# Kernel tuning notes

Hardware: AMD Instinct MI355X
Metric: run time of the kernel (lower is better)

Reference implementation:

```python
import jax, jax.numpy as jnp
import numpy as np

NUM_HEADS = 12
HEAD_DIM = 64


def setup_inputs() -> dict:
    key = jax.random.key(0)
    ks = jax.random.split(key, 4)
    B, T, C = 2, 2048, 768
    x = jax.random.normal(ks[0], (B, T, C), dtype=jnp.float32)
    attention_mask = jnp.ones((B, 1, 1, T), dtype=jnp.int32)
    W_attn = jax.random.normal(ks[1], (C, 3 * C), dtype=jnp.float32) * 0.02
    b_attn = jnp.zeros((3 * C,), dtype=jnp.float32)
    W_proj = jax.random.normal(ks[2], (C, C), dtype=jnp.float32) * 0.02
    b_proj = jnp.zeros((C,), dtype=jnp.float32)
    return {"x": x, "attention_mask": attention_mask, "W_attn": W_attn,
            "b_attn": b_attn, "W_proj": W_proj, "b_proj": b_proj}


def reference(x, attention_mask, W_attn, b_attn, W_proj, b_proj):
    B, T, C = x.shape
    H, D = NUM_HEADS, HEAD_DIM
    # c_attn (Conv1D): y = x @ W + b -> [B, T, 3C]
    qkv = x @ W_attn + b_attn
    q, k, v = jnp.split(qkv, 3, axis=-1)
    # [B, T, C] -> [B, H, T, D]
    q = q.reshape(B, T, H, D).transpose(0, 2, 1, 3)
    k = k.reshape(B, T, H, D).transpose(0, 2, 1, 3)
    v = v.reshape(B, T, H, D).transpose(0, 2, 1, 3)
    scores = jnp.einsum('bhqd,bhkd->bhqk', q, k) / jnp.sqrt(jnp.float32(D))
    causal = jnp.tril(jnp.ones((T, T), dtype=bool))[None, None]  # [1,1,T,T]
    mask_value = jnp.finfo(scores.dtype).min
    scores = jnp.where(causal, scores, mask_value)
    scores = jnp.where(attention_mask == 0, -jnp.inf, scores)
    probs = jax.nn.softmax(scores, axis=-1)
    attn_out = jnp.einsum('bhqk,bhkd->bhqd', probs, v)
    attn_out = attn_out.transpose(0, 2, 1, 3).reshape(B, T, C)
    return attn_out @ W_proj + b_proj
```

## Files before the change

### kernel.cpp

```cpp
#include <hip/hip_runtime.h>

typedef __attribute__((ext_vector_type(8))) short bf16x8;
typedef __attribute__((ext_vector_type(4))) float f32x4;
typedef __attribute__((ext_vector_type(16))) float f32x16;

#define MFMA16(a, b, c) __builtin_amdgcn_mfma_f32_16x16x32_bf16(a, b, c, 0, 0, 0)
#define MFMA32(a, b, c) __builtin_amdgcn_mfma_f32_32x32x16_bf16(a, b, c, 0, 0, 0)
#define LOG2E 1.4426950408889634f

#define BB 2
#define TT 2048
#define CC 768
#define HH 12
#define DD 64
#define MM (BB * TT)
#define N1 (3 * CC)

#define BH_STRIDE 131072

static __device__ __forceinline__ unsigned short f2bf(float f) {
  union { float f; unsigned u; } v; v.f = f;
  unsigned r = (v.u + 0x7FFFu + ((v.u >> 16) & 1u)) >> 16;
  return (unsigned short)r;
}

static __device__ __forceinline__ unsigned cvt_pk_bf16(float lo, float hi) {
  unsigned r;
  asm("v_cvt_pk_bf16_f32 %0, %1, %2" : "=v"(r) : "v"(lo), "v"(hi));
  return r;
}

static __device__ __forceinline__ void gload_lds16(const void* g, void* l) {
  __builtin_amdgcn_global_load_lds(
      (const __attribute__((address_space(1))) void*)g,
      (__attribute__((address_space(3))) void*)l, 16, 0, 0);
}

__global__ __launch_bounds__(256) void k_cvt(const float* __restrict__ x,
                                             unsigned short* __restrict__ o) {
  int i = blockIdx.x * 256 + threadIdx.x;
  float4 v = reinterpret_cast<const float4*>(x)[i];
  ushort4 r;
  r.x = f2bf(v.x); r.y = f2bf(v.y); r.z = f2bf(v.z); r.w = f2bf(v.w);
  reinterpret_cast<ushort4*>(o)[i] = r;
}

__global__ __launch_bounds__(128) void k_mbits(const int* __restrict__ mask,
                                               unsigned int* __restrict__ mb) {
  int i = threadIdx.x;
  unsigned bits = 0;
  const int* p = mask + i * 32;
#pragma unroll
  for (int j = 0; j < 32; ++j) bits |= (p[j] != 0 ? 1u : 0u) << j;
  mb[i] = bits;
}

__global__ __launch_bounds__(256) void k_tr(const float* __restrict__ W,
                                            unsigned short* __restrict__ Wt,
                                            int K, int N) {
  __shared__ float tile[32][33];
  int tx = threadIdx.x, ty = threadIdx.y;
  int n0 = blockIdx.x * 32, k0 = blockIdx.y * 32;
#pragma unroll
  for (int i = 0; i < 4; ++i)
    tile[ty + i * 8][tx] = W[(size_t)(k0 + ty + i * 8) * N + n0 + tx];
  __syncthreads();
#pragma unroll
  for (int i = 0; i < 4; ++i)
    Wt[(size_t)(n0 + ty + i * 8) * K + k0 + tx] = f2bf(tile[tx][ty + i * 8]);
}

template <int MODE>
__global__ __launch_bounds__(256) void k_gemm(
    const unsigned short* __restrict__ A, const unsigned short* __restrict__ Bt,
    const float* __restrict__ bias, float* __restrict__ Cout, int N, int K,
    unsigned short* __restrict__ Qb, unsigned short* __restrict__ Kb,
    unsigned short* __restrict__ Vt) {
  __shared__ __align__(16) unsigned short As[128 * 32];
  __shared__ __align__(16) unsigned short Bs[128 * 32];
  const int tid = threadIdx.x;
  const int lane = tid & 63;
  const int wid = tid >> 6;
  const int l15 = lane & 15, l4 = lane >> 4;
  const int wr = wid >> 1, wc = wid & 1;
  const int brow = blockIdx.x * 128, bcol = blockIdx.y * 128;

  f32x4 acc[4][4] = {};

  const int u0 = tid, u1 = tid + 256;
  const int row0 = u0 >> 2, c0 = (u0 & 3) * 8;
  const int row1 = u1 >> 2, c1 = (u1 & 3) * 8;

  const unsigned short* ga0 = A + (size_t)(brow + row0) * K + c0;
  const unsigned short* ga1 = A + (size_t)(brow + row1) * K + c1;
  const unsigned short* gb0 = Bt + (size_t)(bcol + row0) * K + c0;
  const unsigned short* gb1 = Bt + (size_t)(bcol + row1) * K + c1;
  unsigned short* la0 = As + u0 * 8;
  unsigned short* la1 = As + u1 * 8;
  unsigned short* lb0 = Bs + u0 * 8;
  unsigned short* lb1 = Bs + u1 * 8;

  const int NK = K / 32;
  for (int ks = 0; ks < NK; ++ks) {
    if (ks) __syncthreads();
    const int ko = ks * 32;
    gload_lds16(ga0 + ko, la0);
    gload_lds16(ga1 + ko, la1);
    gload_lds16(gb0 + ko, lb0);
    gload_lds16(gb1 + ko, lb1);
    __syncthreads();
    bf16x8 af[4], bfr[4];
#pragma unroll
    for (int mi = 0; mi < 4; ++mi)
      af[mi] = *reinterpret_cast<const bf16x8*>(&As[(wr * 64 + mi * 16 + l15) * 32 + l4 * 8]);
#pragma unroll
    for (int ni = 0; ni < 4; ++ni)
      bfr[ni] = *reinterpret_cast<const bf16x8*>(&Bs[(wc * 64 + ni * 16 + l15) * 32 + l4 * 8]);
#pragma unroll
    for (int mi = 0; mi < 4; ++mi)
#pragma unroll
      for (int ni = 0; ni < 4; ++ni)
        acc[mi][ni] = MFMA16(af[mi], bfr[ni], acc[mi][ni]);
  }

#pragma unroll
  for (int mi = 0; mi < 4; ++mi) {
    const int m0 = brow + wr * 64 + mi * 16 + l4 * 4;
#pragma unroll
    for (int ni = 0; ni < 4; ++ni) {
      const int n = bcol + wc * 64 + ni * 16 + l15;
      const float bv = bias[n];
      if (MODE == 0) {
#pragma unroll
        for (int r = 0; r < 4; ++r)
          Cout[(size_t)(m0 + r) * N + n] = acc[mi][ni][r] + bv;
      } else {
        const int sec = n / CC;
        const int nn = n - sec * CC;
        const int hh = nn >> 6, d = nn & 63;
        const int b = m0 >> 11;
        const int t0 = m0 & 2047;
        const size_t hbase = (size_t)(b * HH + hh) * BH_STRIDE;
        if (sec == 0) {
#pragma unroll
          for (int r = 0; r < 4; ++r) {
            const int t = t0 + r;
            Qb[hbase + ((t >> 5) * 4 + (d >> 4)) * 512 + (t & 31) * 16 + (d & 15)] =
                f2bf((acc[mi][ni][r] + bv) * 0.125f);
          }
        } else if (sec == 1) {
#pragma unroll
          for (int r = 0; r < 4; ++r) {
            const int t = t0 + r;
            Kb[hbase + ((t >> 5) * 4 + (d >> 4)) * 512 + (t & 31) * 16 + (d & 15)] =
                f2bf(acc[mi][ni][r] + bv);
          }
        } else {
          ushort4 pk;
          pk.x = f2bf(acc[mi][ni][0] + bv);
          pk.y = f2bf(acc[mi][ni][1] + bv);
          pk.z = f2bf(acc[mi][ni][2] + bv);
          pk.w = f2bf(acc[mi][ni][3] + bv);
          *reinterpret_cast<ushort4*>(
              &Vt[hbase + ((t0 >> 6) * 4 + ((t0 >> 4) & 3)) * 1024 + d * 16 + (t0 & 15)]) = pk;
        }
      }
    }
  }
}

__device__ __forceinline__ void loadk(bf16x8 (&dst)[2][4], const unsigned short* Kh,
                                      int kv0, int lo) {
  const unsigned short* kp = Kh + (kv0 >> 5) * 2048 + lo;
#pragma unroll
  for (int kg = 0; kg < 2; ++kg)
#pragma unroll
    for (int dg = 0; dg < 4; ++dg)
      dst[kg][dg] = *reinterpret_cast<const bf16x8*>(&kp[kg * 2048 + dg * 512]);
}

__device__ __forceinline__ void attn_tile(
    int kv0, const bf16x8 (&kf)[2][4], uint2 mb, const bf16x8 (&qf)[4],
    const unsigned short* __restrict__ Vh, int q0, int l31, int h, int lo,
    f32x16& o0, f32x16& o1, float& mrow, float& lrow) {
  const unsigned short* vp = Vh + (kv0 >> 6) * 4096 + lo;
  bf16x8 vf0[4], vf1[4];
#pragma unroll
  for (int kc = 0; kc < 4; ++kc) {
    vf0[kc] = *reinterpret_cast<const bf16x8*>(&vp[kc * 1024]);
    vf1[kc] = *reinterpret_cast<const bf16x8*>(&vp[kc * 1024 + 512]);
  }

  f32x16 s0 = {}, s1 = {};
#pragma unroll
  for (int dg = 0; dg < 4; ++dg) s0 = MFMA32(kf[0][dg], qf[dg], s0);
#pragma unroll
  for (int dg = 0; dg < 4; ++dg) s1 = MFMA32(kf[1][dg], qf[dg], s1);

  if ((mb.x & mb.y) != 0xffffffffu) {
#pragma unroll
    for (int r = 0; r < 16; ++r) {
      const int ki = (r & 3) + 8 * (r >> 2) + 4 * h;
      if (!((mb.x >> ki) & 1u)) s0[r] = -1e30f;
      if (!((mb.y >> ki) & 1u)) s1[r] = -1e30f;
    }
  }
  if (kv0 + 63 > q0) {
    const int q = q0 + l31;
#pragma unroll
    for (int r = 0; r < 16; ++r) {
      const int ki = kv0 + (r & 3) + 8 * (r >> 2) + 4 * h;
      if (ki > q) s0[r] = -1e30f;
      if (ki + 32 > q) s1[r] = -1e30f;
    }
  }

  float tm[8];
#pragma unroll
  for (int r = 0; r < 8; ++r)
    tm[r] = fmaxf(fmaxf(s0[2 * r], s0[2 * r + 1]), fmaxf(s1[2 * r], s1[2 * r + 1]));
  float pmax = fmaxf(fmaxf(fmaxf(tm[0], tm[1]), fmaxf(tm[2], tm[3])),
                     fmaxf(fmaxf(tm[4], tm[5]), fmaxf(tm[6], tm[7])));
  pmax = fmaxf(pmax, __shfl_xor(pmax, 32));

  if (!__all(pmax - mrow <= 8.0f)) {
    const float mnew = fmaxf(mrow, pmax);
    const float al = __builtin_amdgcn_exp2f((mrow - mnew) * LOG2E);
    lrow *= al;
    mrow = mnew;
#pragma unroll
    for (int r = 0; r < 16; ++r) {
      const float ab = __shfl(al, (r & 3) + 8 * (r >> 2) + 4 * h);
      o0[r] *= ab;
      o1[r] *= ab;
    }
  }

  const float ml = mrow * LOG2E;
#pragma unroll
  for (int r = 0; r < 16; ++r) {
    s0[r] = __builtin_amdgcn_exp2f(__builtin_fmaf(s0[r], LOG2E, -ml));
    s1[r] = __builtin_amdgcn_exp2f(__builtin_fmaf(s1[r], LOG2E, -ml));
  }
  float ts[8];
#pragma unroll
  for (int r = 0; r < 8; ++r)
    ts[r] = (s0[2 * r] + s0[2 * r + 1]) + (s1[2 * r] + s1[2 * r + 1]);
  float ps = ((ts[0] + ts[1]) + (ts[2] + ts[3])) + ((ts[4] + ts[5]) + (ts[6] + ts[7]));
  ps += __shfl_xor(ps, 32);
  lrow += ps;

  unsigned pk0[4][2], pk1[4][2];
#pragma unroll
  for (int m = 0; m < 4; ++m)
#pragma unroll
    for (int j = 0; j < 2; ++j) {
      pk0[m][j] = cvt_pk_bf16(s0[4 * m + 2 * j], s0[4 * m + 2 * j + 1]);
      pk1[m][j] = cvt_pk_bf16(s1[4 * m + 2 * j], s1[4 * m + 2 * j + 1]);
    }

#pragma unroll
  for (int kc = 0; kc < 4; ++kc) {
    const unsigned (&pkk)[4][2] = (kc < 2) ? pk0 : pk1;
    const int c1 = (kc & 1) * 2;
    const unsigned v0 = h ? pkk[c1][0] : pkk[c1 + 1][0];
    const unsigned v1 = h ? pkk[c1][1] : pkk[c1 + 1][1];
    const unsigned r0 = (unsigned)__shfl_xor((int)v0, 32);
    const unsigned r1 = (unsigned)__shfl_xor((int)v1, 32);
    union { unsigned u[4]; bf16x8 v; } af;
    af.u[0] = h ? r0 : pkk[c1][0];
    af.u[1] = h ? r1 : pkk[c1][1];
    af.u[2] = h ? pkk[c1 + 1][0] : r0;
    af.u[3] = h ? pkk[c1 + 1][1] : r1;
    o0 = MFMA32(af.v, vf0[kc], o0);
    o1 = MFMA32(af.v, vf1[kc], o1);
  }
}

__global__ __launch_bounds__(64, 2) void k_attn(
    const unsigned short* __restrict__ Q, const unsigned short* __restrict__ Kb,
    const unsigned short* __restrict__ Vt, const unsigned int* __restrict__ mbits,
    float* __restrict__ pO, float* __restrict__ pM, float* __restrict__ pL) {
  const int lane = threadIdx.x;
  const int l31 = lane & 31;
  const int h = lane >> 5;
  const int lo = l31 * 16 + h * 8;
  const int f = blockIdx.x;
  const int xcd = f & 7;
  const int j = f >> 3;
  const int hl = j % 3;
  const int cidx = j / 3;
  const int bh = xcd * 3 + hl;
  int qb, c;
  if (cidx < 64)       { qb = 63 - (cidx >> 2); c = cidx & 3; }
  else if (cidx < 112) { const int u = cidx - 64;  qb = 47 - u / 3;    c = u % 3; }
  else if (cidx < 144) { const int u = cidx - 112; qb = 31 - (u >> 1); c = u & 1; }
  else                 { qb = 15 - (cidx - 144); c = 0; }
  int cb;
  if (qb < 16)      cb = qb;
  else if (qb < 32) cb = 16 + 2 * (qb - 16);
  else if (qb < 48) cb = 48 + 3 * (qb - 32);
  else              cb = 96 + 4 * (qb - 48);
  const int pidx = bh * 160 + cb + c;

  const int b = bh / HH;
  const int q0 = qb * 32;
  const int nt = qb / 2 + 1;
  const int t0 = c * 8;
  const int t1 = (t0 + 8 < nt) ? t0 + 8 : nt;

  const unsigned short* Qh = Q + (size_t)bh * BH_STRIDE;
  const unsigned short* Kh = Kb + (size_t)bh * BH_STRIDE;
  const unsigned short* Vh = Vt + (size_t)bh * BH_STRIDE;
  const unsigned int* mbp = mbits + b * 64;

  bf16x8 qf[4];
  {
    const unsigned short* qp = Qh + (q0 >> 5) * 2048 + lo;
#pragma unroll
    for (int dg = 0; dg < 4; ++dg)
      qf[dg] = *reinterpret_cast<const bf16x8*>(&qp[dg * 512]);
  }

  f32x16 o0 = {}, o1 = {};
  float mrow = -1e30f, lrow = 0.f;

  bf16x8 kfA[2][4], kfB[2][4];
  uint2 mbA, mbB;
  loadk(kfA, Kh, t0 * 64, lo);
  mbA = *reinterpret_cast<const uint2*>(&mbp[t0 * 2]);

  int t = t0;
  while (true) {
    if (t + 1 < t1) {
      loadk(kfB, Kh, (t + 1) * 64, lo);
      mbB = *reinterpret_cast<const uint2*>(&mbp[(t + 1) * 2]);
    }
    attn_tile(t * 64, kfA, mbA, qf, Vh, q0, l31, h, lo, o0, o1, mrow, lrow);
    ++t; if (t >= t1) break;
    if (t + 1 < t1) {
      loadk(kfA, Kh, (t + 1) * 64, lo);
      mbA = *reinterpret_cast<const uint2*>(&mbp[(t + 1) * 2]);
    }
    attn_tile(t * 64, kfB, mbB, qf, Vh, q0, l31, h, lo, o0, o1, mrow, lrow);
    ++t; if (t >= t1) break;
  }

  float* po = pO + (size_t)pidx * 2048;
#pragma unroll
  for (int r = 0; r < 16; ++r) {
    const int crow = (r & 3) + 8 * (r >> 2) + 4 * h;
    po[crow * 64 + l31] = o0[r];
    po[crow * 64 + 32 + l31] = o1[r];
  }
  if (lane < 32) {
    pM[pidx * 32 + lane] = mrow;
    pL[pidx * 32 + lane] = lrow;
  }
}

__global__ __launch_bounds__(256) void k_merge(
    const float* __restrict__ pO, const float* __restrict__ pM,
    const float* __restrict__ pL, unsigned short* __restrict__ AO) {
  const int qb = blockIdx.x, bh = blockIdx.y;
  const int b = bh / HH, hd = bh - b * HH;
  const int nt = qb / 2 + 1;
  const int nch = (nt + 7) >> 3;
  int cb;
  if (qb < 16)      cb = qb;
  else if (qb < 32) cb = 16 + 2 * (qb - 16);
  else if (qb < 48) cb = 48 + 3 * (qb - 32);
  else              cb = 96 + 4 * (qb - 48);
  const int p0 = bh * 160 + cb;

  const int q = threadIdx.x >> 3;
  const int d0 = (threadIdx.x & 7) * 8;

  float mv[4], lv[4];
#pragma unroll
  for (int c = 0; c < 4; ++c) {
    if (c < nch) {
      mv[c] = pM[(p0 + c) * 32 + q];
      lv[c] = pL[(p0 + c) * 32 + q];
    } else {
      mv[c] = -3e38f;
      lv[c] = 0.f;
    }
  }
  const float mst = fmaxf(fmaxf(mv[0], mv[1]), fmaxf(mv[2], mv[3]));
  float sc[4], lst = 0.f;
#pragma unroll
  for (int c = 0; c < 4; ++c) {
    sc[c] = __builtin_amdgcn_exp2f((mv[c] - mst) * LOG2E);
    lst += lv[c] * sc[c];
  }
  const float inv = 1.0f / lst;

  float acc[8] = {};
#pragma unroll
  for (int c = 0; c < 4; ++c) {
    if (c < nch) {
      const float* po = pO + ((size_t)(p0 + c) * 32 + q) * 64 + d0;
      const float4 a = *reinterpret_cast<const float4*>(po);
      const float4 bq = *reinterpret_cast<const float4*>(po + 4);
      acc[0] += sc[c] * a.x; acc[1] += sc[c] * a.y;
      acc[2] += sc[c] * a.z; acc[3] += sc[c] * a.w;
      acc[4] += sc[c] * bq.x; acc[5] += sc[c] * bq.y;
      acc[6] += sc[c] * bq.z; acc[7] += sc[c] * bq.w;
    }
  }
  union { unsigned short u[8]; uint4 v; } ov;
#pragma unroll
  for (int jj = 0; jj < 8; ++jj) ov.u[jj] = f2bf(acc[jj] * inv);
  *reinterpret_cast<uint4*>(&AO[(size_t)(b * TT + qb * 32 + q) * CC + hd * DD + d0]) = ov.v;
}

extern "C" void kernel_launch(void* const* d_in, const int* in_sizes, int n_in,
                              void* d_out, int out_size, void* d_ws, size_t ws_size,
                              hipStream_t stream) {
  const float* x   = (const float*)d_in[0];
  const int* mask  = (const int*)d_in[1];
  const float* Wa  = (const float*)d_in[2];
  const float* ba  = (const float*)d_in[3];
  const float* Wp  = (const float*)d_in[4];
  const float* bp  = (const float*)d_in[5];
  float* out = (float*)d_out;

  char* ws = (char*)d_ws;
  unsigned short* Xb  = (unsigned short*)(ws);
  unsigned short* WaT = (unsigned short*)(ws + 6291456);
  unsigned short* WpT = (unsigned short*)(ws + 9830400);
  unsigned short* Qb  = (unsigned short*)(ws + 11010048);
  unsigned short* Kb  = (unsigned short*)(ws + 17301504);
  unsigned short* Vt  = (unsigned short*)(ws + 23592960);
  unsigned short* AO  = (unsigned short*)(ws + 29884416);
  unsigned int*   Mb  = (unsigned int*)(ws + 36175872);
  float*          pM  = (float*)(ws + 36176384);
  float*          pL  = (float*)(ws + 36667904);
  float*          pO  = (float*)(ws + 37159424);

  k_cvt<<<dim3((MM * CC) / 4 / 256), dim3(256), 0, stream>>>(x, Xb);
  k_mbits<<<dim3(1), dim3(128), 0, stream>>>(mask, Mb);
  k_tr<<<dim3(N1 / 32, CC / 32), dim3(32, 8), 0, stream>>>(Wa, WaT, CC, N1);
  k_tr<<<dim3(CC / 32, CC / 32), dim3(32, 8), 0, stream>>>(Wp, WpT, CC, CC);

  k_gemm<1><<<dim3(MM / 128, N1 / 128), dim3(256), 0, stream>>>(
      Xb, WaT, ba, nullptr, N1, CC, Qb, Kb, Vt);

  k_attn<<<dim3(3840), dim3(64), 0, stream>>>(Qb, Kb, Vt, Mb, pO, pM, pL);
  k_merge<<<dim3(64, BB * HH), dim3(256), 0, stream>>>(pO, pM, pL, AO);

  k_gemm<0><<<dim3(MM / 128, CC / 128), dim3(256), 0, stream>>>(
      AO, WpT, bp, out, CC, CC, nullptr, nullptr, nullptr);
}
```

Before: 97.05 us.

## Fuse prep kernels, triple-buffer GEMM with swizzled LDS, write unsplit attention directly

Merges the input conversion, weight transposes and mask-bit kernels into one launch to cut launch overhead. The GEMM gets a three-stage LDS ring buffer with prefetch two tiles ahead, an XOR swizzle against bank conflicts, and setprio around the MFMA block, so global loads overlap compute. Attention blocks that cover the whole key range now normalize and write bf16 output directly, and the merge kernel only handles the split query blocks. This triples GEMM LDS use, which may lower occupancy, and adds branching in the attention epilogue.

```diff
diff --git a/kernel.cpp b/kernel.cpp
--- a/kernel.cpp
+++ b/kernel.cpp
@@ -15,7 +15,6 @@
 #define DD 64
 #define MM (BB * TT)
 #define N1 (3 * CC)
-
 #define BH_STRIDE 131072
 
 static __device__ __forceinline__ unsigned short f2bf(float f) {
@@ -36,38 +35,48 @@
       (__attribute__((address_space(3))) void*)l, 16, 0, 0);
 }
 
-__global__ __launch_bounds__(256) void k_cvt(const float* __restrict__ x,
-                                             unsigned short* __restrict__ o) {
-  int i = blockIdx.x * 256 + threadIdx.x;
-  float4 v = reinterpret_cast<const float4*>(x)[i];
-  ushort4 r;
-  r.x = f2bf(v.x); r.y = f2bf(v.y); r.z = f2bf(v.z); r.w = f2bf(v.w);
-  reinterpret_cast<ushort4*>(o)[i] = r;
-}
-
-__global__ __launch_bounds__(128) void k_mbits(const int* __restrict__ mask,
-                                               unsigned int* __restrict__ mb) {
-  int i = threadIdx.x;
-  unsigned bits = 0;
-  const int* p = mask + i * 32;
-#pragma unroll
-  for (int j = 0; j < 32; ++j) bits |= (p[j] != 0 ? 1u : 0u) << j;
-  mb[i] = bits;
-}
-
-__global__ __launch_bounds__(256) void k_tr(const float* __restrict__ W,
-                                            unsigned short* __restrict__ Wt,
-                                            int K, int N) {
+#define PREP_CVT 3072
+#define PREP_TR1 1728
+#define PREP_TR2 576
+__global__ __launch_bounds__(256) void k_prep(
+    const float* __restrict__ x, unsigned short* __restrict__ Xb,
+    const float* __restrict__ Wa, unsigned short* __restrict__ WaT,
+    const float* __restrict__ Wp, unsigned short* __restrict__ WpT,
+    const int* __restrict__ mask, unsigned int* __restrict__ mb) {
   __shared__ float tile[32][33];
-  int tx = threadIdx.x, ty = threadIdx.y;
-  int n0 = blockIdx.x * 32, k0 = blockIdx.y * 32;
-#pragma unroll
-  for (int i = 0; i < 4; ++i)
-    tile[ty + i * 8][tx] = W[(size_t)(k0 + ty + i * 8) * N + n0 + tx];
-  __syncthreads();
-#pragma unroll
-  for (int i = 0; i < 4; ++i)
-    Wt[(size_t)(n0 + ty + i * 8) * K + k0 + tx] = f2bf(tile[tx][ty + i * 8]);
+  const int bid = blockIdx.x;
+  const int tid = threadIdx.x;
+  if (bid < PREP_CVT) {
+    const int i = bid * 256 + tid;
+    float4 v = reinterpret_cast<const float4*>(x)[i];
+    ushort4 r;
+    r.x = f2bf(v.x); r.y = f2bf(v.y); r.z = f2bf(v.z); r.w = f2bf(v.w);
+    reinterpret_cast<ushort4*>(Xb)[i] = r;
+  } else if (bid < PREP_CVT + PREP_TR1 + PREP_TR2) {
+    const bool first = bid < PREP_CVT + PREP_TR1;
+    const int b = first ? bid - PREP_CVT : bid - PREP_CVT - PREP_TR1;
+    const int nb = first ? 72 : 24;
+    const int N = first ? N1 : CC;
+    const float* W = first ? Wa : Wp;
+    unsigned short* Wt = first ? WaT : WpT;
+    const int n0 = (b % nb) * 32, k0 = (b / nb) * 32;
+    const int tx = tid & 31, ty = tid >> 5;
+#pragma unroll
+    for (int i = 0; i < 4; ++i)
+      tile[ty + i * 8][tx] = W[(size_t)(k0 + ty + i * 8) * N + n0 + tx];
+    __syncthreads();
+#pragma unroll
+    for (int i = 0; i < 4; ++i)
+      Wt[(size_t)(n0 + ty + i * 8) * CC + k0 + tx] = f2bf(tile[tx][ty + i * 8]);
+  } else {
+    if (tid < 128) {
+      unsigned bits = 0;
+      const int* p = mask + tid * 32;
+#pragma unroll
+      for (int j = 0; j < 32; ++j) bits |= (p[j] != 0 ? 1u : 0u) << j;
+      mb[tid] = bits;
+    }
+  }
 }
 
 template <int MODE>
@@ -76,8 +85,8 @@
     const float* __restrict__ bias, float* __restrict__ Cout, int N, int K,
     unsigned short* __restrict__ Qb, unsigned short* __restrict__ Kb,
     unsigned short* __restrict__ Vt) {
-  __shared__ __align__(16) unsigned short As[128 * 32];
-  __shared__ __align__(16) unsigned short Bs[128 * 32];
+  __shared__ __align__(16) unsigned short As[3][128 * 32];
+  __shared__ __align__(16) unsigned short Bs[3][128 * 32];
   const int tid = threadIdx.x;
   const int lane = tid & 63;
   const int wid = tid >> 6;
@@ -87,41 +96,75 @@
 
   f32x4 acc[4][4] = {};
 
-  const int u0 = tid, u1 = tid + 256;
-  const int row0 = u0 >> 2, c0 = (u0 & 3) * 8;
-  const int row1 = u1 >> 2, c1 = (u1 & 3) * 8;
-
-  const unsigned short* ga0 = A + (size_t)(brow + row0) * K + c0;
-  const unsigned short* ga1 = A + (size_t)(brow + row1) * K + c1;
-  const unsigned short* gb0 = Bt + (size_t)(bcol + row0) * K + c0;
-  const unsigned short* gb1 = Bt + (size_t)(bcol + row1) * K + c1;
-  unsigned short* la0 = As + u0 * 8;
-  unsigned short* la1 = As + u1 * 8;
-  unsigned short* lb0 = Bs + u0 * 8;
-  unsigned short* lb1 = Bs + u1 * 8;
-
-  const int NK = K / 32;
-  for (int ks = 0; ks < NK; ++ks) {
-    if (ks) __syncthreads();
-    const int ko = ks * 32;
-    gload_lds16(ga0 + ko, la0);
-    gload_lds16(ga1 + ko, la1);
-    gload_lds16(gb0 + ko, lb0);
-    gload_lds16(gb1 + ko, lb1);
-    __syncthreads();
+  const int srow = tid >> 2;
+  const int usrc = (tid & 3) ^ ((tid >> 3) & 3);
+  const unsigned short* gA0 = A + (size_t)(brow + srow) * K + usrc * 8;
+  const unsigned short* gA1 = gA0 + (size_t)64 * K;
+  const unsigned short* gB0 = Bt + (size_t)(bcol + srow) * K + usrc * 8;
+  const unsigned short* gB1 = gB0 + (size_t)64 * K;
+  const int dslot = tid * 8;
+
+  const int NT = K / 32;
+
+#define STAGE(t, buf)                                      \
+  do {                                                     \
+    const int ko = (t) * 32;                               \
+    gload_lds16(gA0 + ko, &As[buf][dslot]);                \
+    gload_lds16(gA1 + ko, &As[buf][dslot + 2048]);         \
+    gload_lds16(gB0 + ko, &Bs[buf][dslot]);                \
+    gload_lds16(gB1 + ko, &Bs[buf][dslot + 2048]);         \
+  } while (0)
+
+  const int swz = (l4 ^ ((l15 >> 1) & 3)) * 8;
+  const int arow = wr * 64 + l15;
+  const int brow2 = wc * 64 + l15;
+
+  STAGE(0, 0);
+  STAGE(1, 1);
+
+  int cur = 0;
+  for (int t = 0; t < NT - 1; ++t) {
+    asm volatile("s_waitcnt vmcnt(4)" ::: "memory");
+    __builtin_amdgcn_s_barrier();
+    if (t + 2 < NT) {
+      int nb = cur + 2; if (nb >= 3) nb -= 3;
+      STAGE(t + 2, nb);
+    }
     bf16x8 af[4], bfr[4];
 #pragma unroll
     for (int mi = 0; mi < 4; ++mi)
-      af[mi] = *reinterpret_cast<const bf16x8*>(&As[(wr * 64 + mi * 16 + l15) * 32 + l4 * 8]);
+      af[mi] = *reinterpret_cast<const bf16x8*>(&As[cur][(arow + mi * 16) * 32 + swz]);
 #pragma unroll
     for (int ni = 0; ni < 4; ++ni)
-      bfr[ni] = *reinterpret_cast<const bf16x8*>(&Bs[(wc * 64 + ni * 16 + l15) * 32 + l4 * 8]);
+      bfr[ni] = *reinterpret_cast<const bf16x8*>(&Bs[cur][(brow2 + ni * 16) * 32 + swz]);
+    __builtin_amdgcn_s_setprio(1);
 #pragma unroll
     for (int mi = 0; mi < 4; ++mi)
 #pragma unroll
       for (int ni = 0; ni < 4; ++ni)
         acc[mi][ni] = MFMA16(af[mi], bfr[ni], acc[mi][ni]);
-  }
+    __builtin_amdgcn_s_setprio(0);
+    cur = (cur == 2) ? 0 : cur + 1;
+  }
+  asm volatile("s_waitcnt vmcnt(0)" ::: "memory");
+  __builtin_amdgcn_s_barrier();
+  {
+    bf16x8 af[4], bfr[4];
+#pragma unroll
+    for (int mi = 0; mi < 4; ++mi)
+      af[mi] = *reinterpret_cast<const bf16x8*>(&As[cur][(arow + mi * 16) * 32 + swz]);
+#pragma unroll
+    for (int ni = 0; ni < 4; ++ni)
+      bfr[ni] = *reinterpret_cast<const bf16x8*>(&Bs[cur][(brow2 + ni * 16) * 32 + swz]);
+    __builtin_amdgcn_s_setprio(1);
+#pragma unroll
+    for (int mi = 0; mi < 4; ++mi)
+#pragma unroll
+      for (int ni = 0; ni < 4; ++ni)
+        acc[mi][ni] = MFMA16(af[mi], bfr[ni], acc[mi][ni]);
+    __builtin_amdgcn_s_setprio(0);
+  }
+#undef STAGE
 
 #pragma unroll
   for (int mi = 0; mi < 4; ++mi) {
@@ -280,7 +323,8 @@
 __global__ __launch_bounds__(64, 2) void k_attn(
     const unsigned short* __restrict__ Q, const unsigned short* __restrict__ Kb,
     const unsigned short* __restrict__ Vt, const unsigned int* __restrict__ mbits,
-    float* __restrict__ pO, float* __restrict__ pM, float* __restrict__ pL) {
+    float* __restrict__ pO, float* __restrict__ pM, float* __restrict__ pL,
+    unsigned short* __restrict__ AO) {
   const int lane = threadIdx.x;
   const int l31 = lane & 31;
   const int h = lane >> 5;
@@ -304,6 +348,7 @@
   const int pidx = bh * 160 + cb + c;
 
   const int b = bh / HH;
+  const int hd = bh - b * HH;
   const int q0 = qb * 32;
   const int nt = qb / 2 + 1;
   const int t0 = c * 8;
@@ -346,29 +391,40 @@
     ++t; if (t >= t1) break;
   }
 
-  float* po = pO + (size_t)pidx * 2048;
-#pragma unroll
-  for (int r = 0; r < 16; ++r) {
-    const int crow = (r & 3) + 8 * (r >> 2) + 4 * h;
-    po[crow * 64 + l31] = o0[r];
-    po[crow * 64 + 32 + l31] = o1[r];
-  }
-  if (lane < 32) {
-    pM[pidx * 32 + lane] = mrow;
-    pL[pidx * 32 + lane] = lrow;
+  if (t0 == 0 && t1 == nt) {
+    const float rl = 1.0f / lrow;
+#pragma unroll
+    for (int r = 0; r < 16; ++r) {
+      const int crow = (r & 3) + 8 * (r >> 2) + 4 * h;
+      const float rb = __shfl(rl, crow);
+      const size_t base = (size_t)(b * TT + q0 + crow) * CC + hd * DD;
+      AO[base + l31] = f2bf(o0[r] * rb);
+      AO[base + 32 + l31] = f2bf(o1[r] * rb);
+    }
+  } else {
+    float* po = pO + (size_t)pidx * 2048;
+#pragma unroll
+    for (int r = 0; r < 16; ++r) {
+      const int crow = (r & 3) + 8 * (r >> 2) + 4 * h;
+      po[crow * 64 + l31] = o0[r];
+      po[crow * 64 + 32 + l31] = o1[r];
+    }
+    if (lane < 32) {
+      pM[pidx * 32 + lane] = mrow;
+      pL[pidx * 32 + lane] = lrow;
+    }
   }
 }
 
 __global__ __launch_bounds__(256) void k_merge(
     const float* __restrict__ pO, const float* __restrict__ pM,
     const float* __restrict__ pL, unsigned short* __restrict__ AO) {
-  const int qb = blockIdx.x, bh = blockIdx.y;
+  const int qb = 16 + blockIdx.x, bh = blockIdx.y;
   const int b = bh / HH, hd = bh - b * HH;
   const int nt = qb / 2 + 1;
   const int nch = (nt + 7) >> 3;
   int cb;
-  if (qb < 16)      cb = qb;
-  else if (qb < 32) cb = 16 + 2 * (qb - 16);
+  if (qb < 32)      cb = 16 + 2 * (qb - 16);
   else if (qb < 48) cb = 48 + 3 * (qb - 32);
   else              cb = 96 + 4 * (qb - 48);
   const int p0 = bh * 160 + cb;
@@ -439,16 +495,14 @@
   float*          pL  = (float*)(ws + 36667904);
   float*          pO  = (float*)(ws + 37159424);
 
-  k_cvt<<<dim3((MM * CC) / 4 / 256), dim3(256), 0, stream>>>(x, Xb);
-  k_mbits<<<dim3(1), dim3(128), 0, stream>>>(mask, Mb);
-  k_tr<<<dim3(N1 / 32, CC / 32), dim3(32, 8), 0, stream>>>(Wa, WaT, CC, N1);
-  k_tr<<<dim3(CC / 32, CC / 32), dim3(32, 8), 0, stream>>>(Wp, WpT, CC, CC);
+  k_prep<<<dim3(PREP_CVT + PREP_TR1 + PREP_TR2 + 1), dim3(256), 0, stream>>>(
+      x, Xb, Wa, WaT, Wp, WpT, mask, Mb);
 
   k_gemm<1><<<dim3(MM / 128, N1 / 128), dim3(256), 0, stream>>>(
       Xb, WaT, ba, nullptr, N1, CC, Qb, Kb, Vt);
 
-  k_attn<<<dim3(3840), dim3(64), 0, stream>>>(Qb, Kb, Vt, Mb, pO, pM, pL);
-  k_merge<<<dim3(64, BB * HH), dim3(256), 0, stream>>>(pO, pM, pL, AO);
+  k_attn<<<dim3(3840), dim3(64), 0, stream>>>(Qb, Kb, Vt, Mb, pO, pM, pL, AO);
+  k_merge<<<dim3(48, BB * HH), dim3(256), 0, stream>>>(pO, pM, pL, AO);
 
   k_gemm<0><<<dim3(MM / 128, CC / 128), dim3(256), 0, stream>>>(
       AO, WpT, bp, out, CC, CC, nullptr, nullptr, nullptr);
```

Result: faster. 89.61 us (-7.7%).
